# Optimization experiments

Measured on AMD Instinct MI355X. Metric: run time of the kernel, lower is better.

Reference implementation:

```python
import jax, jax.numpy as jnp
import numpy as np
from jax import lax


def _fuse_proj(proj2):
    # proj2: [B,2,4,4]; slot0 extrinsic E, slot1 intrinsic K. New matrix = E with
    # top 3 rows replaced by K[:3,:3] @ E[:3,:4] (matches the torch in-place update).
    E = proj2[:, 0]
    K = proj2[:, 1, :3, :3]
    top = jnp.einsum('bij,bjk->bik', K, E[:, :3, :4])  # [B,3,4]
    return jnp.concatenate([top, E[:, 3:, :]], axis=1)  # [B,4,4]


def _bilinear_sample(fea, px, py):
    # fea: [B,C,H,W]; px,py: [B,N] pixel coords (align_corners=True), zeros padding.
    B, C, H, W = fea.shape
    x0f = jnp.floor(px); y0f = jnp.floor(py)
    wx1 = px - x0f; wx0 = 1.0 - wx1
    wy1 = py - y0f; wy0 = 1.0 - wy1
    fea_flat = fea.reshape(B, C, H * W)

    def gather(xi, yi):
        valid = (xi >= 0) & (xi <= W - 1) & (yi >= 0) & (yi <= H - 1)
        xc = jnp.clip(xi, 0, W - 1).astype(jnp.int32)
        yc = jnp.clip(yi, 0, H - 1).astype(jnp.int32)
        idx = yc * W + xc  # [B,N]
        v = jnp.take_along_axis(fea_flat, idx[:, None, :], axis=2)  # [B,C,N]
        return v * valid[:, None, :].astype(fea.dtype)

    out = (gather(x0f, y0f) * (wx0 * wy0)[:, None]
           + gather(x0f + 1, y0f) * (wx1 * wy0)[:, None]
           + gather(x0f, y0f + 1) * (wx0 * wy1)[:, None]
           + gather(x0f + 1, y0f + 1) * (wx1 * wy1)[:, None])
    return out  # [B,C,N]


def _homo_warping(src_fea, src_proj, ref_proj, depth_values):
    # src_fea [B,C,H,W], projs [B,4,4], depth_values [B,D] -> [B,C,D,H,W]
    B, C, H, W = src_fea.shape
    D = depth_values.shape[1]
    proj = src_proj @ jnp.linalg.inv(ref_proj)
    rot = proj[:, :3, :3]
    trans = proj[:, :3, 3]  # [B,3]
    ys, xs = jnp.meshgrid(jnp.arange(H, dtype=src_fea.dtype),
                          jnp.arange(W, dtype=src_fea.dtype), indexing='ij')
    xyz = jnp.stack([xs.ravel(), ys.ravel(),
                     jnp.ones(H * W, dtype=src_fea.dtype)])  # [3,HW]
    rot_xyz = jnp.einsum('bij,jn->bin', rot, xyz)  # [B,3,HW]
    proj_xyz = (rot_xyz[:, :, None, :] * depth_values[:, None, :, None]
                + trans[:, :, None, None])  # [B,3,D,HW]
    px = (proj_xyz[:, 0] / proj_xyz[:, 2]).reshape(B, -1)  # [B,D*HW]
    py = (proj_xyz[:, 1] / proj_xyz[:, 2]).reshape(B, -1)
    warped = _bilinear_sample(src_fea, px, py)  # [B,C,D*HW]
    return warped.reshape(B, C, D, H, W)


def _depth_regression(p, depth_values):
    # p [B,D,H,W], depth_values [B,D] -> [B,H,W]
    return jnp.sum(p * depth_values[:, :, None, None], axis=1)


def setup_inputs() -> dict:
    key = jax.random.key(0)
    k1, k2 = jax.random.split(key)
    B, V, C, D, H, W = 1, 3, 32, 96, 128, 160
    features = jax.random.normal(k1, (V, B, C, H, W), jnp.float32)
    K = np.eye(4, dtype=np.float32)
    K[0, 0] = 200.0; K[1, 1] = 200.0; K[0, 2] = W / 2.0; K[1, 2] = H / 2.0
    projs = np.zeros((B, V, 2, 4, 4), np.float32)
    for v in range(V):
        E = np.eye(4, dtype=np.float32)
        E[0, 3] = 0.1 * v  # small x-baseline per source view
        projs[:, v, 0] = E
        projs[:, v, 1] = K
    proj_matrices = jnp.asarray(projs)
    depth_values = jnp.broadcast_to(
        jnp.linspace(425.0, 935.0, D, dtype=jnp.float32)[None], (B, D))
    reg_weight = jax.random.normal(k2, (1, C, 3, 3, 3), jnp.float32) * 0.05
    reg_bias = jnp.zeros((1,), jnp.float32)
    return {'features': features, 'proj_matrices': proj_matrices,
            'depth_values': depth_values, 'reg_weight': reg_weight,
            'reg_bias': reg_bias, 'num_depth': D}


def reference(features, proj_matrices, depth_values, reg_weight, reg_bias, num_depth):
    V = features.shape[0]
    B, C, H, W = features.shape[1:]
    D = num_depth
    ref_fea = features[0]
    ref_proj_new = _fuse_proj(proj_matrices[:, 0])
    # ref volume + per-view warped volumes -> sum and sum of squares
    ref_volume = ref_fea[:, :, None, :, :]  # broadcast over D
    volume_sum = jnp.broadcast_to(ref_volume, (B, C, D, H, W))
    volume_sq_sum = volume_sum ** 2
    for v in range(1, V):
        src_proj_new = _fuse_proj(proj_matrices[:, v])
        warped = _homo_warping(features[v], src_proj_new, ref_proj_new, depth_values)
        volume_sum = volume_sum + warped
        volume_sq_sum = volume_sq_sum + warped ** 2
    volume_variance = volume_sq_sum / V - (volume_sum / V) ** 2  # [B,C,D,H,W]
    # cost regularization: Conv3d C->1, k=3, SAME
    cost_reg = lax.conv_general_dilated(
        volume_variance, reg_weight, window_strides=(1, 1, 1), padding='SAME',
        dimension_numbers=('NCDHW', 'OIDHW', 'NCDHW'))
    cost_reg = cost_reg + reg_bias[None, :, None, None, None]
    prob_volume_pre = cost_reg[:, 0]  # [B,D,H,W]
    prob_volume = jax.nn.softmax(prob_volume_pre, axis=1)
    depth = _depth_regression(prob_volume, depth_values)  # [B,H,W]
    # photometric confidence (no-grad branch): sliding sum of 4 along depth
    prob_sum4 = lax.reduce_window(
        prob_volume, 0.0, lax.add, window_dimensions=(1, 4, 1, 1),
        window_strides=(1, 1, 1, 1), padding=((0, 0), (1, 2), (0, 0), (0, 0)))
    idx_f = _depth_regression(prob_volume, jnp.broadcast_to(
        jnp.arange(D, dtype=prob_volume.dtype)[None], (B, D)))
    depth_index = jnp.clip(idx_f.astype(jnp.int32), 0, D - 1)  # [B,H,W]
    photometric_confidence = jnp.take_along_axis(
        prob_sum4, depth_index[:, None], axis=1)[:, 0]  # [B,H,W]
    return depth, photometric_confidence
```

## Files before the change

### kernel.cpp

```cpp
#include <hip/hip_runtime.h>
#include <math.h>

#define W_ 160
#define H_ 128
#define C_ 32
#define D_ 96
#define NPIX (H_*W_)

#define OFF_PART    0
#define OFF_WT      5898240
#define OFF_ROT     5899104
#define OFF_VAR_BYTES  23596544ull
#define VAR_BYTES      125829120ull

typedef unsigned int uint;

__device__ inline uint pack2(float a, float b) {
    unsigned short ua = __builtin_bit_cast(unsigned short, (_Float16)a);
    unsigned short ub = __builtin_bit_cast(unsigned short, (_Float16)b);
    return (uint)ua | ((uint)ub << 16);
}
__device__ inline float f16lo(uint u){ return (float)__builtin_bit_cast(_Float16,(unsigned short)(u & 0xffffu)); }
__device__ inline float f16hi(uint u){ return (float)__builtin_bit_cast(_Float16,(unsigned short)(u >> 16)); }

__global__ __launch_bounds__(256) void k_prep(
    const float* __restrict__ proj,
    const float* __restrict__ wsrc,
    float* __restrict__ wT,
    float* __restrict__ rotrans)
{
    int t = threadIdx.x;
    for (int i = t; i < 864; i += 256) {
        int s = i >> 5, c = i & 31;
        wT[i] = wsrc[c * 27 + s];
    }
    if (t == 0) {
        float P[3][16];
        for (int v = 0; v < 3; ++v) {
            const float* E = proj + v * 32;
            const float* K = proj + v * 32 + 16;
            for (int i = 0; i < 3; ++i)
                for (int j = 0; j < 4; ++j)
                    P[v][i*4+j] = K[i*4+0]*E[0*4+j] + K[i*4+1]*E[1*4+j] + K[i*4+2]*E[2*4+j];
            for (int j = 0; j < 4; ++j) P[v][12+j] = E[12+j];
        }
        const float* m = P[0];
        float inv[16];
        inv[0]  =  m[5]*m[10]*m[15] - m[5]*m[11]*m[14] - m[9]*m[6]*m[15] + m[9]*m[7]*m[14] + m[13]*m[6]*m[11] - m[13]*m[7]*m[10];
        inv[4]  = -m[4]*m[10]*m[15] + m[4]*m[11]*m[14] + m[8]*m[6]*m[15] - m[8]*m[7]*m[14] - m[12]*m[6]*m[11] + m[12]*m[7]*m[10];
        inv[8]  =  m[4]*m[9]*m[15]  - m[4]*m[11]*m[13] - m[8]*m[5]*m[15] + m[8]*m[7]*m[13] + m[12]*m[5]*m[11] - m[12]*m[7]*m[9];
        inv[12] = -m[4]*m[9]*m[14]  + m[4]*m[10]*m[13] + m[8]*m[5]*m[14] - m[8]*m[6]*m[13] - m[12]*m[5]*m[10] + m[12]*m[6]*m[9];
        inv[1]  = -m[1]*m[10]*m[15] + m[1]*m[11]*m[14] + m[9]*m[2]*m[15] - m[9]*m[3]*m[14] - m[13]*m[2]*m[11] + m[13]*m[3]*m[10];
        inv[5]  =  m[0]*m[10]*m[15] - m[0]*m[11]*m[14] - m[8]*m[2]*m[15] + m[8]*m[3]*m[14] + m[12]*m[2]*m[11] - m[12]*m[3]*m[10];
        inv[9]  = -m[0]*m[9]*m[15]  + m[0]*m[11]*m[13] + m[8]*m[1]*m[15] - m[8]*m[3]*m[13] - m[12]*m[1]*m[11] + m[12]*m[3]*m[9];
        inv[13] =  m[0]*m[9]*m[14]  - m[0]*m[10]*m[13] - m[8]*m[1]*m[14] + m[8]*m[2]*m[13] + m[12]*m[1]*m[10] - m[12]*m[2]*m[9];
        inv[2]  =  m[1]*m[6]*m[15]  - m[1]*m[7]*m[14]  - m[5]*m[2]*m[15] + m[5]*m[3]*m[14] + m[13]*m[2]*m[7]  - m[13]*m[3]*m[6];
        inv[6]  = -m[0]*m[6]*m[15]  + m[0]*m[7]*m[14]  + m[4]*m[2]*m[15] - m[4]*m[3]*m[14] - m[12]*m[2]*m[7]  + m[12]*m[3]*m[6];
        inv[10] =  m[0]*m[5]*m[15]  - m[0]*m[7]*m[13]  - m[4]*m[1]*m[15] + m[4]*m[3]*m[13] + m[12]*m[1]*m[7]  - m[12]*m[3]*m[5];
        inv[14] = -m[0]*m[5]*m[14]  + m[0]*m[6]*m[13]  + m[4]*m[1]*m[14] - m[4]*m[2]*m[13] - m[12]*m[1]*m[6]  + m[12]*m[2]*m[5];
        inv[3]  = -m[1]*m[6]*m[11]  + m[1]*m[7]*m[10]  + m[5]*m[2]*m[11] - m[5]*m[3]*m[10] - m[9]*m[2]*m[7]   + m[9]*m[3]*m[6];
        inv[7]  =  m[0]*m[6]*m[11]  - m[0]*m[7]*m[10]  - m[4]*m[2]*m[11] + m[4]*m[3]*m[10] + m[8]*m[2]*m[7]   - m[8]*m[3]*m[6];
        inv[11] = -m[0]*m[5]*m[11]  + m[0]*m[7]*m[9]   + m[4]*m[1]*m[11] - m[4]*m[3]*m[9]  - m[8]*m[1]*m[7]   + m[8]*m[3]*m[5];
        inv[15] =  m[0]*m[5]*m[10]  - m[0]*m[6]*m[9]   - m[4]*m[1]*m[10] + m[4]*m[2]*m[9]  + m[8]*m[1]*m[6]   - m[8]*m[2]*m[5];
        float det = m[0]*inv[0] + m[1]*inv[4] + m[2]*inv[8] + m[3]*inv[12];
        float rdet = 1.0f / det;
        for (int i = 0; i < 16; ++i) inv[i] *= rdet;

        for (int v = 1; v < 3; ++v) {
            float M[16];
            for (int i = 0; i < 4; ++i)
                for (int j = 0; j < 4; ++j) {
                    float a = 0.f;
                    for (int k = 0; k < 4; ++k) a += P[v][i*4+k] * inv[k*4+j];
                    M[i*4+j] = a;
                }
            float* o = rotrans + (v-1)*12;
            for (int i = 0; i < 3; ++i) {
                for (int j = 0; j < 3; ++j) o[i*3+j] = M[i*4+j];
                o[9+i] = M[i*4+3];
            }
        }
    }
}

__global__ __launch_bounds__(256) void k_var(
    const float* __restrict__ fea,
    const float* __restrict__ rotrans_g,
    const float* __restrict__ dvals,
    uint* __restrict__ varU)
{
    const int tid = threadIdx.x;
    const int bx = blockIdx.x, by = blockIdx.y, ds = blockIdx.z;
    const int tx = tid & 15, ty = tid >> 4;
    const int gx = bx * 16 + tx, gy = by * 16 + ty;
    const float dv = dvals[ds];

    const int ro = gy * W_ + gx;
    float w[2][4];
    int   off[2][4];
    const float xf = (float)gx, yf = (float)gy;
    #pragma unroll
    for (int v = 0; v < 2; ++v) {
        const float* rt = rotrans_g + v * 12;
        float A0 = rt[0]*xf + rt[1]*yf + rt[2];
        float A1 = rt[3]*xf + rt[4]*yf + rt[5];
        float A2 = rt[6]*xf + rt[7]*yf + rt[8];
        float X = A0 * dv + rt[9];
        float Y = A1 * dv + rt[10];
        float Z = A2 * dv + rt[11];
        float rz = __builtin_amdgcn_rcpf(Z);
        float pxf = X * rz, pyf = Y * rz;
        float x0f = floorf(pxf), y0f = floorf(pyf);
        float fx = pxf - x0f, fy = pyf - y0f;
        float w00 = (1.f-fx)*(1.f-fy), w10 = fx*(1.f-fy);
        float w01 = (1.f-fx)*fy,       w11 = fx*fy;
        float x1f = x0f + 1.f, y1f = y0f + 1.f;
        bool vx0 = (x0f >= 0.f) && (x0f <= (float)(W_-1));
        bool vx1 = (x1f >= 0.f) && (x1f <= (float)(W_-1));
        bool vy0 = (y0f >= 0.f) && (y0f <= (float)(H_-1));
        bool vy1 = (y1f >= 0.f) && (y1f <= (float)(H_-1));
        w[v][0] = (vx0 && vy0) ? w00 : 0.f;
        w[v][1] = (vx1 && vy0) ? w10 : 0.f;
        w[v][2] = (vx0 && vy1) ? w01 : 0.f;
        w[v][3] = (vx1 && vy1) ? w11 : 0.f;
        int xc0 = (int)fminf(fmaxf(x0f, 0.f), (float)(W_-1));
        int xc1 = (int)fminf(fmaxf(x1f, 0.f), (float)(W_-1));
        int yc0 = (int)fminf(fmaxf(y0f, 0.f), (float)(H_-1));
        int yc1 = (int)fminf(fmaxf(y1f, 0.f), (float)(H_-1));
        const int vb = (v + 1) * C_ * NPIX;
        off[v][0] = vb + yc0 * W_ + xc0;
        off[v][1] = vb + yc0 * W_ + xc1;
        off[v][2] = vb + yc1 * W_ + xc0;
        off[v][3] = vb + yc1 * W_ + xc1;
    }

    const float inv3 = 1.f / 3.f;
    uint outv[16];
    #pragma unroll
    for (int c2 = 0; c2 < 16; ++c2) {
        float vr[2];
        #pragma unroll
        for (int h = 0; h < 2; ++h) {
            const float* pc = fea + (size_t)(c2 * 2 + h) * NPIX;
            float s = pc[ro];
            float q = s * s;
            #pragma unroll
            for (int v = 0; v < 2; ++v) {
                float f00 = pc[off[v][0]], f10 = pc[off[v][1]];
                float f01 = pc[off[v][2]], f11 = pc[off[v][3]];
                float wf = w[v][0]*f00 + w[v][1]*f10 + w[v][2]*f01 + w[v][3]*f11;
                s += wf;
                q += wf * wf;
            }
            float mm = s * inv3;
            vr[h] = q * inv3 - mm * mm;
        }
        outv[c2] = pack2(vr[0], vr[1]);
    }
    uint4* dst = (uint4*)(varU + ((size_t)ds * NPIX + gy * W_ + gx) * 16);
    #pragma unroll
    for (int j = 0; j < 4; ++j) dst[j] = ((uint4*)outv)[j];
}

#define HSB 19
#define NHP (18*HSB)
#define PSTR 20

__global__ __launch_bounds__(256) void k_conv(
    const uint* __restrict__ varU,
    const float* __restrict__ wT,
    float* __restrict__ part)
{
    __shared__ uint  sL[NHP * PSTR];
    __shared__ float4 sW[216];

    const int tid = threadIdx.x;
    const int bx = blockIdx.x, by = blockIdx.y, ds = blockIdx.z;

    for (int i = tid; i < 216; i += 256) sW[i] = ((const float4*)wT)[i];
    #pragma unroll
    for (int pi = 0; pi < 2; ++pi) {
        const int p = tid + pi * 256;
        if (p < NHP) {
            const int py = p / HSB;
            const int px = p - py * HSB;
            if (px < 18) {
                const int gy = by * 16 + py - 1;
                const int gx = bx * 16 + px - 1;
                uint4* d = (uint4*)&sL[p * PSTR];
                if (gy < 0 || gy >= H_ || gx < 0 || gx >= W_) {
                    uint4 z = make_uint4(0u,0u,0u,0u);
                    d[0] = z; d[1] = z; d[2] = z; d[3] = z;
                } else {
                    const uint4* g = (const uint4*)(varU + ((size_t)ds * NPIX + gy * W_ + gx) * 16);
                    d[0] = g[0]; d[1] = g[1]; d[2] = g[2]; d[3] = g[3];
                }
            }
        }
    }
    __syncthreads();

    const int ty = tid >> 4, tx = tid & 15;
    float acc[3] = {0.f, 0.f, 0.f};
    #pragma unroll
    for (int c4 = 0; c4 < 8; ++c4) {
        #pragma unroll
        for (int kh = 0; kh < 3; ++kh) {
            float4 wv[3][3];
            #pragma unroll
            for (int kd = 0; kd < 3; ++kd)
                #pragma unroll
                for (int kw = 0; kw < 3; ++kw)
                    wv[kd][kw] = sW[((kd*3 + kh)*3 + kw) * 8 + c4];
            const int rowb = (ty + kh) * HSB + tx;
            #pragma unroll
            for (int kw = 0; kw < 3; ++kw) {
                const uint* u = &sL[(rowb + kw) * PSTR + c4 * 2];
                uint u0 = u[0], u1 = u[1];
                float f0 = f16lo(u0), f1 = f16hi(u0);
                float f2 = f16lo(u1), f3 = f16hi(u1);
                #pragma unroll
                for (int kd = 0; kd < 3; ++kd)
                    acc[kd] += f0*wv[kd][kw].x + f1*wv[kd][kw].y
                             + f2*wv[kd][kw].z + f3*wv[kd][kw].w;
            }
        }
    }
    const int oy = by * 16 + ty;
    const int ox = bx * 16 + tx;
    #pragma unroll
    for (int kd = 0; kd < 3; ++kd)
        part[(size_t)(kd * D_ + ds) * NPIX + oy * W_ + ox] = acc[kd];
}

__global__ __launch_bounds__(256) void k_softmax(
    const float* __restrict__ part,
    const float* __restrict__ dvals,
    const float* __restrict__ bias,
    float* __restrict__ out)
{
    __shared__ float sD[96];
    if (threadIdx.x < 96) sD[threadIdx.x] = dvals[threadIdx.x];
    __syncthreads();

    int pix = blockIdx.x * 256 + threadIdx.x;
    if (pix >= NPIX) return;
    float e[96];
    const float b = bias[0];
    float m = -1e30f;
    #pragma unroll
    for (int d = 0; d < 96; ++d) {
        float c = part[(size_t)(D_ + d) * NPIX + pix];
        if (d > 0)  c += part[(size_t)(d - 1) * NPIX + pix];
        if (d < 95) c += part[(size_t)(2*D_ + d + 1) * NPIX + pix];
        c += b;
        e[d] = c;
        m = fmaxf(m, c);
    }
    float sum = 0.f, dsum = 0.f, isum = 0.f;
    #pragma unroll
    for (int d = 0; d < 96; ++d) {
        float ex = __expf(e[d] - m);
        e[d] = ex;
        sum  += ex;
        dsum += ex * sD[d];
        isum += ex * (float)d;
    }
    float inv = 1.f / sum;
    float depth = dsum * inv;
    float idxf = isum * inv;
    int di = (int)idxf;
    di = di < 0 ? 0 : (di > 95 ? 95 : di);
    float cs = 0.f;
    #pragma unroll
    for (int d = 0; d < 96; ++d) {
        bool in = (d >= di - 1) && (d <= di + 2);
        cs += in ? e[d] : 0.f;
    }
    out[pix] = depth;
    out[NPIX + pix] = cs * inv;
}

extern "C" void kernel_launch(void* const* d_in, const int* in_sizes, int n_in,
                              void* d_out, int out_size, void* d_ws, size_t ws_size,
                              hipStream_t stream)
{
    const float* features = (const float*)d_in[0];
    const float* proj     = (const float*)d_in[1];
    const float* dvals    = (const float*)d_in[2];
    const float* wsrc     = (const float*)d_in[3];
    const float* bias     = (const float*)d_in[4];
    float* ws = (float*)d_ws;
    float* part    = ws + OFF_PART;
    float* wT      = ws + OFF_WT;
    float* rotrans = ws + OFF_ROT;
    uint*  varU    = (uint*)((char*)d_ws + OFF_VAR_BYTES);
    float* out = (float*)d_out;

    hipLaunchKernelGGL(k_prep, dim3(1), dim3(256), 0, stream, proj, wsrc, wT, rotrans);
    hipLaunchKernelGGL(k_var, dim3(10, 8, 96), dim3(256), 0, stream,
                       features, rotrans, dvals, varU);
    hipLaunchKernelGGL(k_conv, dim3(10, 8, 96), dim3(256), 0, stream,
                       varU, wT, part);
    hipLaunchKernelGGL(k_softmax, dim3(80), dim3(256), 0, stream, part, dvals, bias, out);
}
```

Measured before the change: 307.2 us.

## Split variance channels across wavefronts and store var volume in channel-chunk layout

k_var now uses 8x8 pixel tiles, and each of the four wavefronts in a block computes 8 channels for those pixels instead of one thread computing all 32. The intermediate variance buffer changes from 64 bytes per pixel to four channel-chunk planes of 16 bytes each, so every store and load is a single uint4 and adjacent lanes touch contiguous memory. k_conv's halo loader is rewritten to gather the four chunk planes into the same shared-memory layout. This aims to raise parallelism and per-thread register headroom in k_var and to improve store coalescing. The cost is that the projection and bilinear weights are recomputed four times per pixel.

```diff
diff --git a/kernel.cpp b/kernel.cpp
--- a/kernel.cpp
+++ b/kernel.cpp
@@ -91,8 +91,10 @@
 {
     const int tid = threadIdx.x;
     const int bx = blockIdx.x, by = blockIdx.y, ds = blockIdx.z;
-    const int tx = tid & 15, ty = tid >> 4;
-    const int gx = bx * 16 + tx, gy = by * 16 + ty;
+    const int chunk = tid >> 6;
+    const int lane = tid & 63;
+    const int gx = bx * 8 + (lane & 7);
+    const int gy = by * 8 + (lane >> 3);
     const float dv = dvals[ds];
 
     const int ro = gy * W_ + gx;
@@ -135,13 +137,14 @@
     }
 
     const float inv3 = 1.f / 3.f;
-    uint outv[16];
-    #pragma unroll
-    for (int c2 = 0; c2 < 16; ++c2) {
+    uint outv[4];
+    const int c0 = chunk * 8;
+    #pragma unroll
+    for (int j = 0; j < 4; ++j) {
         float vr[2];
         #pragma unroll
         for (int h = 0; h < 2; ++h) {
-            const float* pc = fea + (size_t)(c2 * 2 + h) * NPIX;
+            const float* pc = fea + (size_t)(c0 + 2*j + h) * NPIX;
             float s = pc[ro];
             float q = s * s;
             #pragma unroll
@@ -155,11 +158,10 @@
             float mm = s * inv3;
             vr[h] = q * inv3 - mm * mm;
         }
-        outv[c2] = pack2(vr[0], vr[1]);
-    }
-    uint4* dst = (uint4*)(varU + ((size_t)ds * NPIX + gy * W_ + gx) * 16);
-    #pragma unroll
-    for (int j = 0; j < 4; ++j) dst[j] = ((uint4*)outv)[j];
+        outv[j] = pack2(vr[0], vr[1]);
+    }
+    uint4* dst = (uint4*)(varU + ((size_t)(ds * 4 + chunk) * NPIX + gy * W_ + gx) * 4);
+    *dst = *(uint4*)outv;
 }
 
 #define HSB 19
@@ -178,23 +180,19 @@
     const int bx = blockIdx.x, by = blockIdx.y, ds = blockIdx.z;
 
     for (int i = tid; i < 216; i += 256) sW[i] = ((const float4*)wT)[i];
-    #pragma unroll
-    for (int pi = 0; pi < 2; ++pi) {
-        const int p = tid + pi * 256;
-        if (p < NHP) {
-            const int py = p / HSB;
-            const int px = p - py * HSB;
-            if (px < 18) {
-                const int gy = by * 16 + py - 1;
-                const int gx = bx * 16 + px - 1;
-                uint4* d = (uint4*)&sL[p * PSTR];
-                if (gy < 0 || gy >= H_ || gx < 0 || gx >= W_) {
-                    uint4 z = make_uint4(0u,0u,0u,0u);
-                    d[0] = z; d[1] = z; d[2] = z; d[3] = z;
-                } else {
-                    const uint4* g = (const uint4*)(varU + ((size_t)ds * NPIX + gy * W_ + gx) * 16);
-                    d[0] = g[0]; d[1] = g[1]; d[2] = g[2]; d[3] = g[3];
-                }
+    for (int i = tid; i < NHP * 4; i += 256) {
+        const int chunk = i / NHP;
+        const int p = i - chunk * NHP;
+        const int py = p / HSB;
+        const int px = p - py * HSB;
+        if (px < 18) {
+            const int gy = by * 16 + py - 1;
+            const int gx = bx * 16 + px - 1;
+            uint4* d = (uint4*)&sL[p * PSTR + chunk * 4];
+            if (gy < 0 || gy >= H_ || gx < 0 || gx >= W_) {
+                *d = make_uint4(0u,0u,0u,0u);
+            } else {
+                *d = *(const uint4*)(varU + ((size_t)(ds * 4 + chunk) * NPIX + gy * W_ + gx) * 4);
             }
         }
     }
@@ -298,7 +296,7 @@
     float* out = (float*)d_out;
 
     hipLaunchKernelGGL(k_prep, dim3(1), dim3(256), 0, stream, proj, wsrc, wT, rotrans);
-    hipLaunchKernelGGL(k_var, dim3(10, 8, 96), dim3(256), 0, stream,
+    hipLaunchKernelGGL(k_var, dim3(20, 16, 96), dim3(256), 0, stream,
                        features, rotrans, dvals, varU);
     hipLaunchKernelGGL(k_conv, dim3(10, 8, 96), dim3(256), 0, stream,
                        varU, wT, part);
```

Result: slower. 523.1 us (+70.2%).
